# Performance work log

Measured on AMD Instinct MI355X. Metric: run time of the kernel, lower is better.

Reference implementation:

```python
import jax, jax.numpy as jnp
import numpy as np
import math

D_MODEL = 1024
N_HEADS = 16
D_K = D_MODEL // N_HEADS


def setup_inputs() -> dict:
    key = jax.random.key(0)
    ks = jax.random.split(key, 12)
    B, S, D = 4, 2048, D_MODEL
    scale = 1.0 / math.sqrt(D)
    inp = {
        "q": jax.random.normal(ks[0], (B, S, D), jnp.float32),
        "k": jax.random.normal(ks[1], (B, S, D), jnp.float32),
        "v": jax.random.normal(ks[2], (B, S, D), jnp.float32),
        "w_q": jax.random.normal(ks[3], (D, D), jnp.float32) * scale,
        "b_q": jnp.zeros((D,), jnp.float32),
        "w_k": jax.random.normal(ks[4], (D, D), jnp.float32) * scale,
        "b_k": jnp.zeros((D,), jnp.float32),
        "w_v": jax.random.normal(ks[5], (D, D), jnp.float32) * scale,
        "b_v": jnp.zeros((D,), jnp.float32),
        "w_o": jax.random.normal(ks[6], (D, D), jnp.float32) * scale,
        "b_o": jnp.zeros((D,), jnp.float32),
        "ln_gamma": jnp.ones((D,), jnp.float32),
        "ln_beta": jnp.zeros((D,), jnp.float32),
    }
    return inp


def reference(q, k, v, w_q, b_q, w_k, b_k, w_v, b_v, w_o, b_o, ln_gamma, ln_beta):
    B, Sq, D = q.shape
    Sk = k.shape[1]
    residual = q
    # Projections (torch Linear: x @ W.T + b); split into heads -> [B, H, S, d_k]
    qh = (q @ w_q.T + b_q).reshape(B, Sq, N_HEADS, D_K).transpose(0, 2, 1, 3)
    kh = (k @ w_k.T + b_k).reshape(B, Sk, N_HEADS, D_K).transpose(0, 2, 1, 3)
    vh = (v @ w_v.T + b_v).reshape(B, Sk, N_HEADS, D_K).transpose(0, 2, 1, 3)
    # Scaled dot-product attention (dropout is identity in eval mode)
    scores = jnp.einsum("bhqd,bhkd->bhqk", qh, kh) / jnp.sqrt(jnp.float32(D_K))
    attn = jax.nn.softmax(scores, axis=-1)  # [B, H, Sq, Sk]
    ctx = jnp.einsum("bhqk,bhkd->bhqd", attn, vh)
    ctx = ctx.transpose(0, 2, 1, 3).reshape(B, Sq, D)
    out = ctx @ w_o.T + b_o
    # Post-LN with residual
    x = out + residual
    mu = jnp.mean(x, axis=-1, keepdims=True)
    var = jnp.var(x, axis=-1, keepdims=True)
    out = (x - mu) / jnp.sqrt(var + 1e-5) * ln_gamma + ln_beta
    return out, attn
```

## Files before the change

kernel.cpp:

```cpp
#include <hip/hip_runtime.h>

#define B_ 4
#define S_ 2048
#define D_ 1024
#define H_ 16
#define DK_ 64
#define M_ (B_ * S_)

typedef __attribute__((ext_vector_type(8))) _Float16 f16x8;
typedef __attribute__((ext_vector_type(4))) _Float16 f16x4;
typedef __attribute__((ext_vector_type(4))) float f32x4;

#define QSCALE 0.18033688011113607f

__device__ __forceinline__ f32x4 mfma16(f16x8 a, f16x8 b, f32x4 c) {
  return __builtin_amdgcn_mfma_f32_16x16x32_f16(a, b, c, 0, 0, 0);
}

__device__ __forceinline__ void gl2lds(const _Float16* g, _Float16* l) {
  __builtin_amdgcn_global_load_lds(
      (const __attribute__((address_space(1))) void*)g,
      (__attribute__((address_space(3))) void*)l, 16, 0, 0);
}

#define NW8 (D_ * D_ / 8)
__global__ __launch_bounds__(256) void cvt_w(
    const float* __restrict__ wq, const float* __restrict__ wk,
    const float* __restrict__ wv, const float* __restrict__ wo,
    _Float16* __restrict__ wqh, _Float16* __restrict__ wkh,
    _Float16* __restrict__ wvh, _Float16* __restrict__ woh) {
  const int i = blockIdx.x * 256 + threadIdx.x;
  const int t = i >> 17;
  const int off = i & (NW8 - 1);
  const float* src = t == 0 ? wq : (t == 1 ? wk : (t == 2 ? wv : wo));
  _Float16* dst = t == 0 ? wqh : (t == 1 ? wkh : (t == 2 ? wvh : woh));
  const f32x4 a = *reinterpret_cast<const f32x4*>(&src[(size_t)off * 8]);
  const f32x4 b = *reinterpret_cast<const f32x4*>(&src[(size_t)off * 8 + 4]);
  f16x8 h;
  h[0] = (_Float16)a[0]; h[1] = (_Float16)a[1]; h[2] = (_Float16)a[2]; h[3] = (_Float16)a[3];
  h[4] = (_Float16)b[0]; h[5] = (_Float16)b[1]; h[6] = (_Float16)b[2]; h[7] = (_Float16)b[3];
  *reinterpret_cast<f16x8*>(&dst[(size_t)off * 8]) = h;
}

__global__ __launch_bounds__(256, 2) void gemm_qkv(
    const float* __restrict__ Xq, const float* __restrict__ Xk, const float* __restrict__ Xv,
    const _Float16* __restrict__ Wq, const _Float16* __restrict__ Wk, const _Float16* __restrict__ Wv,
    const float* __restrict__ bq, const float* __restrict__ bk, const float* __restrict__ bv,
    _Float16* __restrict__ Qh, _Float16* __restrict__ Kh, _Float16* __restrict__ Vt) {
  __shared__ _Float16 As[128 * 72];
  __shared__ _Float16 Bs[256 * 64];
  const int third = blockIdx.x >> 8;
  const int bid = blockIdx.x & 255;
  const float* X = third == 0 ? Xq : (third == 1 ? Xk : Xv);
  const _Float16* Bw = third == 0 ? Wq : (third == 1 ? Wk : Wv);
  const float* bias = third == 0 ? bq : (third == 1 ? bk : bv);

  const int t = threadIdx.x;
  const int lane = t & 63;
  const int w = t >> 6;
  const int wr = w >> 1, wc = w & 1;
  const int l15 = lane & 15, g = lane >> 4;
  const int m0 = (bid & 63) * 128;
  const int n0 = (bid >> 6) * 256;

  f32x4 acc[4][8] = {};
  const int srow = lane >> 3;
  const int schk = (lane & 7) * 8;
  const int ar = t >> 4;
  const int ac = (t & 15) * 4;

  for (int kt = 0; kt < 16; ++kt) {
    const int k0 = kt * 64;
#pragma unroll
    for (int u = 0; u < 8; ++u)
      gl2lds(&Bw[(size_t)(n0 + u * 32 + w * 8 + srow) * D_ + k0 + schk], &Bs[u * 2048 + w * 512]);
#pragma unroll
    for (int rg = 0; rg < 8; ++rg) {
      const int r = rg * 16 + ar;
      const f32x4 vv = *reinterpret_cast<const f32x4*>(&X[(size_t)(m0 + r) * D_ + k0 + ac]);
      f16x4 hh;
      hh[0] = (_Float16)vv[0]; hh[1] = (_Float16)vv[1];
      hh[2] = (_Float16)vv[2]; hh[3] = (_Float16)vv[3];
      *reinterpret_cast<f16x4*>(&As[r * 72 + ac]) = hh;
    }
    __syncthreads();
#pragma unroll
    for (int kk = 0; kk < 2; ++kk) {
      f16x8 af[4], bfr[8];
#pragma unroll
      for (int m = 0; m < 4; ++m)
        af[m] = *reinterpret_cast<const f16x8*>(&As[(wr * 64 + m * 16 + l15) * 72 + kk * 32 + 8 * g]);
#pragma unroll
      for (int n = 0; n < 8; ++n)
        bfr[n] = *reinterpret_cast<const f16x8*>(&Bs[(wc * 128 + n * 16 + l15) * 64 + kk * 32 + 8 * g]);
#pragma unroll
      for (int m = 0; m < 4; ++m)
#pragma unroll
        for (int n = 0; n < 8; ++n)
          acc[m][n] = mfma16(af[m], bfr[n], acc[m][n]);
    }
    __syncthreads();
  }

  if (third < 2) {
    _Float16* Y = third == 0 ? Qh : Kh;
    const float scl = third == 0 ? QSCALE : 1.0f;
#pragma unroll
    for (int m = 0; m < 4; ++m)
#pragma unroll
      for (int n = 0; n < 8; ++n)
#pragma unroll
        for (int i = 0; i < 4; ++i) {
          const int R = m0 + wr * 64 + m * 16 + 4 * g + i;
          const int C = n0 + wc * 128 + n * 16 + l15;
          Y[(size_t)R * D_ + C] = (_Float16)((acc[m][n][i] + bias[C]) * scl);
        }
  } else {
#pragma unroll
    for (int m = 0; m < 4; ++m)
#pragma unroll
      for (int n = 0; n < 8; ++n) {
        const int R0 = m0 + wr * 64 + m * 16 + 4 * g;
        const int C = n0 + wc * 128 + n * 16 + l15;
        const int b = R0 >> 11, s0 = R0 & (S_ - 1);
        const int h = C >> 6, dk = C & (DK_ - 1);
        f16x4 hv;
#pragma unroll
        for (int i = 0; i < 4; ++i) hv[i] = (_Float16)(acc[m][n][i] + bias[C]);
        *reinterpret_cast<f16x4*>(&Vt[((size_t)((b * H_ + h) * DK_ + dk)) * S_ + s0]) = hv;
      }
  }
}

__global__ __launch_bounds__(256) void gemm_out(const _Float16* __restrict__ A,
                                                const _Float16* __restrict__ Bw,
                                                const float* __restrict__ bias,
                                                float* __restrict__ out) {
  __shared__ _Float16 As[128 * 64];
  __shared__ _Float16 Bs[128 * 64];
  const int t = threadIdx.x;
  const int lane = t & 63;
  const int w = t >> 6;
  const int wr = w >> 1, wc = w & 1;
  const int l15 = lane & 15, g = lane >> 4;
  const int m0 = (blockIdx.x & 63) * 128;
  const int n0 = (blockIdx.x >> 6) * 128;

  f32x4 acc[4][4] = {};
  const int srow = lane >> 3;
  const int schk = (lane & 7) * 8;

  for (int kt = 0; kt < 16; ++kt) {
    const int k0 = kt * 64;
#pragma unroll
    for (int u = 0; u < 4; ++u) {
      const int r = u * 32 + w * 8 + srow;
      gl2lds(&A[(size_t)(m0 + r) * D_ + k0 + schk], &As[u * 2048 + w * 512]);
      gl2lds(&Bw[(size_t)(n0 + r) * D_ + k0 + schk], &Bs[u * 2048 + w * 512]);
    }
    __syncthreads();
#pragma unroll
    for (int kk = 0; kk < 2; ++kk) {
      f16x8 af[4], bfr[4];
#pragma unroll
      for (int m = 0; m < 4; ++m)
        af[m] = *reinterpret_cast<const f16x8*>(&As[(wr * 64 + m * 16 + l15) * 64 + kk * 32 + 8 * g]);
#pragma unroll
      for (int n = 0; n < 4; ++n)
        bfr[n] = *reinterpret_cast<const f16x8*>(&Bs[(wc * 64 + n * 16 + l15) * 64 + kk * 32 + 8 * g]);
#pragma unroll
      for (int m = 0; m < 4; ++m)
#pragma unroll
        for (int n = 0; n < 4; ++n)
          acc[m][n] = mfma16(af[m], bfr[n], acc[m][n]);
    }
    __syncthreads();
  }

#pragma unroll
  for (int m = 0; m < 4; ++m)
#pragma unroll
    for (int n = 0; n < 4; ++n)
#pragma unroll
      for (int i = 0; i < 4; ++i) {
        const int R = m0 + wr * 64 + m * 16 + 4 * g + i;
        const int C = n0 + wc * 64 + n * 16 + l15;
        out[(size_t)R * D_ + C] = acc[m][n][i] + bias[C];
      }
}

__global__ __launch_bounds__(256) void attn_pass1(const _Float16* __restrict__ Qh,
                                                  const _Float16* __restrict__ Kh,
                                                  float* __restrict__ lbuf) {
  __shared__ float red[4][64];
  const int t = threadIdx.x;
  const int lane = t & 63;
  const int w = t >> 6;
  const int l15 = lane & 15, g = lane >> 4;
  const int qc = blockIdx.x & 31;
  const int bh = blockIdx.x >> 5;
  const int b = bh >> 4, h = bh & 15;
  const int q0 = qc * 64;
  const _Float16* Qp = Qh + (size_t)b * S_ * D_ + h * DK_;
  const _Float16* Kp = Kh + (size_t)b * S_ * D_ + h * DK_;

  f16x8 qa[4][2];
#pragma unroll
  for (int mr = 0; mr < 4; ++mr)
#pragma unroll
    for (int kk = 0; kk < 2; ++kk)
      qa[mr][kk] = *reinterpret_cast<const f16x8*>(&Qp[(size_t)(q0 + mr * 16 + l15) * D_ + kk * 32 + 8 * g]);

  float l[4][4] = {};
  const int cbeg = w * (S_ / 4), cend = cbeg + (S_ / 4);
  f16x8 kb0 = *reinterpret_cast<const f16x8*>(&Kp[(size_t)(cbeg + l15) * D_ + 8 * g]);
  f16x8 kb1 = *reinterpret_cast<const f16x8*>(&Kp[(size_t)(cbeg + l15) * D_ + 32 + 8 * g]);
  for (int c0 = cbeg; c0 < cend; c0 += 16) {
    const int cn = (c0 + 16 < cend) ? c0 + 16 : cbeg;
    const f16x8 nb0 = *reinterpret_cast<const f16x8*>(&Kp[(size_t)(cn + l15) * D_ + 8 * g]);
    const f16x8 nb1 = *reinterpret_cast<const f16x8*>(&Kp[(size_t)(cn + l15) * D_ + 32 + 8 * g]);
#pragma unroll
    for (int mr = 0; mr < 4; ++mr) {
      f32x4 sc = {};
      sc = mfma16(qa[mr][0], kb0, sc);
      sc = mfma16(qa[mr][1], kb1, sc);
#pragma unroll
      for (int i = 0; i < 4; ++i) l[mr][i] += exp2f(sc[i]);
    }
    kb0 = nb0; kb1 = nb1;
  }
#pragma unroll
  for (int mask = 1; mask < 16; mask <<= 1)
#pragma unroll
    for (int mr = 0; mr < 4; ++mr)
#pragma unroll
      for (int i = 0; i < 4; ++i) l[mr][i] += __shfl_xor(l[mr][i], mask, 64);
  if (l15 == 0)
#pragma unroll
    for (int mr = 0; mr < 4; ++mr)
#pragma unroll
      for (int i = 0; i < 4; ++i) red[w][mr * 16 + 4 * g + i] = l[mr][i];
  __syncthreads();
  if (t < 64)
    lbuf[(size_t)bh * S_ + q0 + t] = red[0][t] + red[1][t] + red[2][t] + red[3][t];
}

__global__ __launch_bounds__(256) void attn_pass2(const _Float16* __restrict__ Qh,
                                                  const _Float16* __restrict__ Kh,
                                                  const _Float16* __restrict__ Vt,
                                                  const float* __restrict__ lbuf,
                                                  float* __restrict__ attn,
                                                  _Float16* __restrict__ ctx) {
  __shared__ float Ps[4][32 * 36];
  const int t = threadIdx.x;
  const int lane = t & 63;
  const int w = t >> 6;
  const int l15 = lane & 15, g = lane >> 4;
  const int qc = blockIdx.x & 15;
  const int bh = blockIdx.x >> 4;
  const int b = bh >> 4, h = bh & 15;
  const int q0 = qc * 128 + w * 32;
  const _Float16* Qp = Qh + (size_t)b * S_ * D_ + h * DK_;
  const _Float16* Kp = Kh + (size_t)b * S_ * D_ + h * DK_;
  const _Float16* Vp = Vt + (size_t)bh * DK_ * S_;

  f16x8 qa[2][2];
#pragma unroll
  for (int mr = 0; mr < 2; ++mr)
#pragma unroll
    for (int kk = 0; kk < 2; ++kk)
      qa[mr][kk] = *reinterpret_cast<const f16x8*>(&Qp[(size_t)(q0 + mr * 16 + l15) * D_ + kk * 32 + 8 * g]);

  float il[2][4];
#pragma unroll
  for (int mr = 0; mr < 2; ++mr)
#pragma unroll
    for (int i = 0; i < 4; ++i)
      il[mr][i] = 1.0f / lbuf[(size_t)bh * S_ + q0 + mr * 16 + 4 * g + i];

  f32x4 accv[2][4] = {};
  float* Pw = Ps[w];
  const int sr = lane >> 3;
  const int sc4 = (lane & 7) * 4;

#pragma unroll 2
  for (int c0 = 0; c0 < S_; c0 += 32) {
#pragma unroll
    for (int ct = 0; ct < 2; ++ct) {
      const f16x8 kb0 = *reinterpret_cast<const f16x8*>(&Kp[(size_t)(c0 + ct * 16 + l15) * D_ + 8 * g]);
      const f16x8 kb1 = *reinterpret_cast<const f16x8*>(&Kp[(size_t)(c0 + ct * 16 + l15) * D_ + 32 + 8 * g]);
#pragma unroll
      for (int mr = 0; mr < 2; ++mr) {
        f32x4 sc = {};
        sc = mfma16(qa[mr][0], kb0, sc);
        sc = mfma16(qa[mr][1], kb1, sc);
#pragma unroll
        for (int i = 0; i < 4; ++i)
          Pw[(mr * 16 + 4 * g + i) * 36 + ct * 16 + l15] = exp2f(sc[i]) * il[mr][i];
      }
    }
#pragma unroll
    for (int j = 0; j < 4; ++j) {
      const int r = sr + 8 * j;
      const f32x4 pv = *reinterpret_cast<const f32x4*>(&Pw[r * 36 + sc4]);
      __builtin_nontemporal_store(pv,
          reinterpret_cast<f32x4*>(&attn[((size_t)bh * S_ + q0 + r) * S_ + c0 + sc4]));
    }
#pragma unroll
    for (int mr = 0; mr < 2; ++mr) {
      const f32x4 p0 = *reinterpret_cast<const f32x4*>(&Pw[(mr * 16 + l15) * 36 + 8 * g]);
      const f32x4 p1 = *reinterpret_cast<const f32x4*>(&Pw[(mr * 16 + l15) * 36 + 8 * g + 4]);
      f16x8 pa;
#pragma unroll
      for (int j = 0; j < 4; ++j) { pa[j] = (_Float16)p0[j]; pa[4 + j] = (_Float16)p1[j]; }
#pragma unroll
      for (int n = 0; n < 4; ++n) {
        const f16x8 vb = *reinterpret_cast<const f16x8*>(&Vp[(size_t)(n * 16 + l15) * S_ + c0 + 8 * g]);
        accv[mr][n] = mfma16(pa, vb, accv[mr][n]);
      }
    }
  }
#pragma unroll
  for (int mr = 0; mr < 2; ++mr)
#pragma unroll
    for (int n = 0; n < 4; ++n)
#pragma unroll
      for (int i = 0; i < 4; ++i) {
        const int row = q0 + mr * 16 + 4 * g + i;
        ctx[((size_t)(b * S_ + row)) * D_ + h * DK_ + n * 16 + l15] = (_Float16)accv[mr][n][i];
      }
}

__global__ __launch_bounds__(256) void ln_kernel(float* __restrict__ out,
                                                 const float* __restrict__ resid,
                                                 const float* __restrict__ gamma,
                                                 const float* __restrict__ beta) {
  const int t = threadIdx.x;
  const int lane = t & 63, w = t >> 6;
  const int row = blockIdx.x * 4 + w;
  const size_t rb = (size_t)row * D_;
  f32x4 x[4];
  float s = 0.f, s2 = 0.f;
#pragma unroll
  for (int c = 0; c < 4; ++c) {
    const int off = c * 256 + lane * 4;
    const f32x4 o = *reinterpret_cast<const f32x4*>(&out[rb + off]);
    const f32x4 r = *reinterpret_cast<const f32x4*>(&resid[rb + off]);
    x[c] = o + r;
#pragma unroll
    for (int j = 0; j < 4; ++j) { s += x[c][j]; s2 += x[c][j] * x[c][j]; }
  }
#pragma unroll
  for (int mask = 1; mask < 64; mask <<= 1) {
    s += __shfl_xor(s, mask, 64);
    s2 += __shfl_xor(s2, mask, 64);
  }
  const float mu = s * (1.0f / D_);
  const float var = s2 * (1.0f / D_) - mu * mu;
  const float rstd = rsqrtf(var + 1e-5f);
#pragma unroll
  for (int c = 0; c < 4; ++c) {
    const int off = c * 256 + lane * 4;
    const f32x4 gm = *reinterpret_cast<const f32x4*>(&gamma[off]);
    const f32x4 bt = *reinterpret_cast<const f32x4*>(&beta[off]);
    f32x4 y;
#pragma unroll
    for (int j = 0; j < 4; ++j) y[j] = (x[c][j] - mu) * rstd * gm[j] + bt[j];
    *reinterpret_cast<f32x4*>(&out[rb + off]) = y;
  }
}

extern "C" void kernel_launch(void* const* d_in, const int* in_sizes, int n_in,
                              void* d_out, int out_size, void* d_ws, size_t ws_size,
                              hipStream_t stream) {
  (void)in_sizes; (void)n_in; (void)out_size; (void)ws_size;
  const float* q    = (const float*)d_in[0];
  const float* k    = (const float*)d_in[1];
  const float* v    = (const float*)d_in[2];
  const float* w_q  = (const float*)d_in[3];
  const float* b_q  = (const float*)d_in[4];
  const float* w_k  = (const float*)d_in[5];
  const float* b_k  = (const float*)d_in[6];
  const float* w_v  = (const float*)d_in[7];
  const float* b_v  = (const float*)d_in[8];
  const float* w_o  = (const float*)d_in[9];
  const float* b_o  = (const float*)d_in[10];
  const float* ln_g = (const float*)d_in[11];
  const float* ln_b = (const float*)d_in[12];

  char* ws = (char*)d_ws;
  _Float16* wq_h = (_Float16*)(ws + ((size_t)0 << 20));
  _Float16* wk_h = (_Float16*)(ws + ((size_t)2 << 20));
  _Float16* wv_h = (_Float16*)(ws + ((size_t)4 << 20));
  _Float16* wo_h = (_Float16*)(ws + ((size_t)6 << 20));
  _Float16* Qh   = (_Float16*)(ws + ((size_t)8 << 20));
  _Float16* Kh   = (_Float16*)(ws + ((size_t)26 << 20));
  _Float16* Vt   = (_Float16*)(ws + ((size_t)44 << 20));
  _Float16* ctx  = (_Float16*)(ws + ((size_t)62 << 20));
  float*    lbuf = (float*)(ws + ((size_t)80 << 20));

  float* out_f = (float*)d_out;
  float* attn_f = out_f + (size_t)M_ * D_;

  cvt_w<<<4 * NW8 / 256, 256, 0, stream>>>(w_q, w_k, w_v, w_o, wq_h, wk_h, wv_h, wo_h);

  gemm_qkv<<<768, 256, 0, stream>>>(q, k, v, wq_h, wk_h, wv_h, b_q, b_k, b_v, Qh, Kh, Vt);

  attn_pass1<<<B_ * H_ * (S_ / 64), 256, 0, stream>>>(Qh, Kh, lbuf);
  attn_pass2<<<B_ * H_ * (S_ / 128), 256, 0, stream>>>(Qh, Kh, Vt, lbuf, attn_f, ctx);

  gemm_out<<<512, 256, 0, stream>>>(ctx, wo_h, b_o, out_f);
  ln_kernel<<<M_ / 4, 256, 0, stream>>>(out_f, q, ln_g, ln_b);
}
```

Measured before the change: 489.9 us.

## Fuse attention row-sum pass into main attention kernel and widen output GEMM tile

```diff
diff --git a/kernel.cpp b/kernel.cpp
--- a/kernel.cpp
+++ b/kernel.cpp
@@ -132,46 +132,46 @@
   }
 }
 
-__global__ __launch_bounds__(256) void gemm_out(const _Float16* __restrict__ A,
-                                                const _Float16* __restrict__ Bw,
-                                                const float* __restrict__ bias,
-                                                float* __restrict__ out) {
+__global__ __launch_bounds__(256, 2) void gemm_out(const _Float16* __restrict__ A,
+                                                   const _Float16* __restrict__ Bw,
+                                                   const float* __restrict__ bias,
+                                                   float* __restrict__ out) {
   __shared__ _Float16 As[128 * 64];
-  __shared__ _Float16 Bs[128 * 64];
+  __shared__ _Float16 Bs[256 * 64];
   const int t = threadIdx.x;
   const int lane = t & 63;
   const int w = t >> 6;
   const int wr = w >> 1, wc = w & 1;
   const int l15 = lane & 15, g = lane >> 4;
   const int m0 = (blockIdx.x & 63) * 128;
-  const int n0 = (blockIdx.x >> 6) * 128;
-
-  f32x4 acc[4][4] = {};
+  const int n0 = (blockIdx.x >> 6) * 256;
+
+  f32x4 acc[4][8] = {};
   const int srow = lane >> 3;
   const int schk = (lane & 7) * 8;
 
   for (int kt = 0; kt < 16; ++kt) {
     const int k0 = kt * 64;
 #pragma unroll
-    for (int u = 0; u < 4; ++u) {
-      const int r = u * 32 + w * 8 + srow;
-      gl2lds(&A[(size_t)(m0 + r) * D_ + k0 + schk], &As[u * 2048 + w * 512]);
-      gl2lds(&Bw[(size_t)(n0 + r) * D_ + k0 + schk], &Bs[u * 2048 + w * 512]);
-    }
+    for (int u = 0; u < 4; ++u)
+      gl2lds(&A[(size_t)(m0 + u * 32 + w * 8 + srow) * D_ + k0 + schk], &As[u * 2048 + w * 512]);
+#pragma unroll
+    for (int u = 0; u < 8; ++u)
+      gl2lds(&Bw[(size_t)(n0 + u * 32 + w * 8 + srow) * D_ + k0 + schk], &Bs[u * 2048 + w * 512]);
     __syncthreads();
 #pragma unroll
     for (int kk = 0; kk < 2; ++kk) {
-      f16x8 af[4], bfr[4];
+      f16x8 af[4], bfr[8];
 #pragma unroll
       for (int m = 0; m < 4; ++m)
         af[m] = *reinterpret_cast<const f16x8*>(&As[(wr * 64 + m * 16 + l15) * 64 + kk * 32 + 8 * g]);
 #pragma unroll
-      for (int n = 0; n < 4; ++n)
-        bfr[n] = *reinterpret_cast<const f16x8*>(&Bs[(wc * 64 + n * 16 + l15) * 64 + kk * 32 + 8 * g]);
+      for (int n = 0; n < 8; ++n)
+        bfr[n] = *reinterpret_cast<const f16x8*>(&Bs[(wc * 128 + n * 16 + l15) * 64 + kk * 32 + 8 * g]);
 #pragma unroll
       for (int m = 0; m < 4; ++m)
 #pragma unroll
-        for (int n = 0; n < 4; ++n)
+        for (int n = 0; n < 8; ++n)
           acc[m][n] = mfma16(af[m], bfr[n], acc[m][n]);
     }
     __syncthreads();
@@ -180,78 +180,22 @@
 #pragma unroll
   for (int m = 0; m < 4; ++m)
 #pragma unroll
-    for (int n = 0; n < 4; ++n)
+    for (int n = 0; n < 8; ++n)
 #pragma unroll
       for (int i = 0; i < 4; ++i) {
         const int R = m0 + wr * 64 + m * 16 + 4 * g + i;
-        const int C = n0 + wc * 64 + n * 16 + l15;
+        const int C = n0 + wc * 128 + n * 16 + l15;
         out[(size_t)R * D_ + C] = acc[m][n][i] + bias[C];
       }
 }
 
-__global__ __launch_bounds__(256) void attn_pass1(const _Float16* __restrict__ Qh,
-                                                  const _Float16* __restrict__ Kh,
-                                                  float* __restrict__ lbuf) {
-  __shared__ float red[4][64];
-  const int t = threadIdx.x;
-  const int lane = t & 63;
-  const int w = t >> 6;
-  const int l15 = lane & 15, g = lane >> 4;
-  const int qc = blockIdx.x & 31;
-  const int bh = blockIdx.x >> 5;
-  const int b = bh >> 4, h = bh & 15;
-  const int q0 = qc * 64;
-  const _Float16* Qp = Qh + (size_t)b * S_ * D_ + h * DK_;
-  const _Float16* Kp = Kh + (size_t)b * S_ * D_ + h * DK_;
-
-  f16x8 qa[4][2];
-#pragma unroll
-  for (int mr = 0; mr < 4; ++mr)
-#pragma unroll
-    for (int kk = 0; kk < 2; ++kk)
-      qa[mr][kk] = *reinterpret_cast<const f16x8*>(&Qp[(size_t)(q0 + mr * 16 + l15) * D_ + kk * 32 + 8 * g]);
-
-  float l[4][4] = {};
-  const int cbeg = w * (S_ / 4), cend = cbeg + (S_ / 4);
-  f16x8 kb0 = *reinterpret_cast<const f16x8*>(&Kp[(size_t)(cbeg + l15) * D_ + 8 * g]);
-  f16x8 kb1 = *reinterpret_cast<const f16x8*>(&Kp[(size_t)(cbeg + l15) * D_ + 32 + 8 * g]);
-  for (int c0 = cbeg; c0 < cend; c0 += 16) {
-    const int cn = (c0 + 16 < cend) ? c0 + 16 : cbeg;
-    const f16x8 nb0 = *reinterpret_cast<const f16x8*>(&Kp[(size_t)(cn + l15) * D_ + 8 * g]);
-    const f16x8 nb1 = *reinterpret_cast<const f16x8*>(&Kp[(size_t)(cn + l15) * D_ + 32 + 8 * g]);
-#pragma unroll
-    for (int mr = 0; mr < 4; ++mr) {
-      f32x4 sc = {};
-      sc = mfma16(qa[mr][0], kb0, sc);
-      sc = mfma16(qa[mr][1], kb1, sc);
-#pragma unroll
-      for (int i = 0; i < 4; ++i) l[mr][i] += exp2f(sc[i]);
-    }
-    kb0 = nb0; kb1 = nb1;
-  }
-#pragma unroll
-  for (int mask = 1; mask < 16; mask <<= 1)
-#pragma unroll
-    for (int mr = 0; mr < 4; ++mr)
-#pragma unroll
-      for (int i = 0; i < 4; ++i) l[mr][i] += __shfl_xor(l[mr][i], mask, 64);
-  if (l15 == 0)
-#pragma unroll
-    for (int mr = 0; mr < 4; ++mr)
-#pragma unroll
-      for (int i = 0; i < 4; ++i) red[w][mr * 16 + 4 * g + i] = l[mr][i];
-  __syncthreads();
-  if (t < 64)
-    lbuf[(size_t)bh * S_ + q0 + t] = red[0][t] + red[1][t] + red[2][t] + red[3][t];
-}
-
-__global__ __launch_bounds__(256) void attn_pass2(const _Float16* __restrict__ Qh,
+__global__ __launch_bounds__(256) void attn_fused(const _Float16* __restrict__ Qh,
                                                   const _Float16* __restrict__ Kh,
                                                   const _Float16* __restrict__ Vt,
-                                                  const float* __restrict__ lbuf,
                                                   float* __restrict__ attn,
                                                   _Float16* __restrict__ ctx) {
   __shared__ float Ps[4][32 * 36];
+  __shared__ float red[4][128];
   const int t = threadIdx.x;
   const int lane = t & 63;
   const int w = t >> 6;
@@ -259,24 +203,67 @@
   const int qc = blockIdx.x & 15;
   const int bh = blockIdx.x >> 4;
   const int b = bh >> 4, h = bh & 15;
-  const int q0 = qc * 128 + w * 32;
+  const int q0b = qc * 128;
+  const int q0 = q0b + w * 32;
   const _Float16* Qp = Qh + (size_t)b * S_ * D_ + h * DK_;
   const _Float16* Kp = Kh + (size_t)b * S_ * D_ + h * DK_;
   const _Float16* Vp = Vt + (size_t)bh * DK_ * S_;
 
+  {
+    f16x8 qaA[8][2];
+#pragma unroll
+    for (int mr = 0; mr < 8; ++mr)
+#pragma unroll
+      for (int kk = 0; kk < 2; ++kk)
+        qaA[mr][kk] = *reinterpret_cast<const f16x8*>(&Qp[(size_t)(q0b + mr * 16 + l15) * D_ + kk * 32 + 8 * g]);
+
+    float l[8][4] = {};
+    const int cbeg = w * (S_ / 4), cend = cbeg + (S_ / 4);
+    f16x8 kb0 = *reinterpret_cast<const f16x8*>(&Kp[(size_t)(cbeg + l15) * D_ + 8 * g]);
+    f16x8 kb1 = *reinterpret_cast<const f16x8*>(&Kp[(size_t)(cbeg + l15) * D_ + 32 + 8 * g]);
+    for (int c0 = cbeg; c0 < cend; c0 += 16) {
+      const int cn = (c0 + 16 < cend) ? c0 + 16 : cbeg;
+      const f16x8 nb0 = *reinterpret_cast<const f16x8*>(&Kp[(size_t)(cn + l15) * D_ + 8 * g]);
+      const f16x8 nb1 = *reinterpret_cast<const f16x8*>(&Kp[(size_t)(cn + l15) * D_ + 32 + 8 * g]);
+#pragma unroll
+      for (int mr = 0; mr < 8; ++mr) {
+        f32x4 sc = {};
+        sc = mfma16(qaA[mr][0], kb0, sc);
+        sc = mfma16(qaA[mr][1], kb1, sc);
+#pragma unroll
+        for (int i = 0; i < 4; ++i) l[mr][i] += exp2f(sc[i]);
+      }
+      kb0 = nb0; kb1 = nb1;
+    }
+#pragma unroll
+    for (int mask = 1; mask < 16; mask <<= 1)
+#pragma unroll
+      for (int mr = 0; mr < 8; ++mr)
+#pragma unroll
+        for (int i = 0; i < 4; ++i) l[mr][i] += __shfl_xor(l[mr][i], mask, 64);
+    if (l15 == 0)
+#pragma unroll
+      for (int mr = 0; mr < 8; ++mr)
+#pragma unroll
+        for (int i = 0; i < 4; ++i) red[w][mr * 16 + 4 * g + i] = l[mr][i];
+  }
+  __syncthreads();
+
+  float il[2][4];
+#pragma unroll
+  for (int mr = 0; mr < 2; ++mr)
+#pragma unroll
+    for (int i = 0; i < 4; ++i) {
+      const int rl = w * 32 + mr * 16 + 4 * g + i;
+      il[mr][i] = 1.0f / (red[0][rl] + red[1][rl] + red[2][rl] + red[3][rl]);
+    }
+
   f16x8 qa[2][2];
 #pragma unroll
   for (int mr = 0; mr < 2; ++mr)
 #pragma unroll
     for (int kk = 0; kk < 2; ++kk)
       qa[mr][kk] = *reinterpret_cast<const f16x8*>(&Qp[(size_t)(q0 + mr * 16 + l15) * D_ + kk * 32 + 8 * g]);
-
-  float il[2][4];
-#pragma unroll
-  for (int mr = 0; mr < 2; ++mr)
-#pragma unroll
-    for (int i = 0; i < 4; ++i)
-      il[mr][i] = 1.0f / lbuf[(size_t)bh * S_ + q0 + mr * 16 + 4 * g + i];
 
   f32x4 accv[2][4] = {};
   float* Pw = Ps[w];
@@ -303,8 +290,7 @@
     for (int j = 0; j < 4; ++j) {
       const int r = sr + 8 * j;
       const f32x4 pv = *reinterpret_cast<const f32x4*>(&Pw[r * 36 + sc4]);
-      __builtin_nontemporal_store(pv,
-          reinterpret_cast<f32x4*>(&attn[((size_t)bh * S_ + q0 + r) * S_ + c0 + sc4]));
+      *reinterpret_cast<f32x4*>(&attn[((size_t)bh * S_ + q0 + r) * S_ + c0 + sc4]) = pv;
     }
 #pragma unroll
     for (int mr = 0; mr < 2; ++mr) {
@@ -397,7 +383,6 @@
   _Float16* Kh   = (_Float16*)(ws + ((size_t)26 << 20));
   _Float16* Vt   = (_Float16*)(ws + ((size_t)44 << 20));
   _Float16* ctx  = (_Float16*)(ws + ((size_t)62 << 20));
-  float*    lbuf = (float*)(ws + ((size_t)80 << 20));
 
   float* out_f = (float*)d_out;
   float* attn_f = out_f + (size_t)M_ * D_;
@@ -406,9 +391,8 @@
 
   gemm_qkv<<<768, 256, 0, stream>>>(q, k, v, wq_h, wk_h, wv_h, b_q, b_k, b_v, Qh, Kh, Vt);
 
-  attn_pass1<<<B_ * H_ * (S_ / 64), 256, 0, stream>>>(Qh, Kh, lbuf);
-  attn_pass2<<<B_ * H_ * (S_ / 128), 256, 0, stream>>>(Qh, Kh, Vt, lbuf, attn_f, ctx);
-
-  gemm_out<<<512, 256, 0, stream>>>(ctx, wo_h, b_o, out_f);
+  attn_fused<<<B_ * H_ * (S_ / 128), 256, 0, stream>>>(Qh, Kh, Vt, attn_f, ctx);
+
+  gemm_out<<<256, 256, 0, stream>>>(ctx, wo_h, b_o, out_f);
   ln_kernel<<<M_ / 4, 256, 0, stream>>>(out_f, q, ln_g, ln_b);
 }
```

Result: slower. 677.2 us (+38.2%).
